# Kernel tuning notes

Hardware: AMD Instinct MI355X
Metric: run time of the kernel (lower is better)

## Reference

```python
import jax, jax.numpy as jnp
import numpy as np
from jax import lax

B_IDX = 0  # label_vocab['B']
E_IDX = 1  # label_vocab['E']
NEG = -10000.0


def setup_inputs() -> dict:
    key = jax.random.key(0)
    k1, k2 = jax.random.split(key)
    B, T, L = 256, 512, 64
    X = jax.random.normal(k1, (B, T, L), dtype=jnp.float32)
    transition = jax.random.normal(k2, (L, L), dtype=jnp.float32)
    # __init__ masking: no transitions out of 'E', none into 'B'
    transition = transition.at[E_IDX, :].set(NEG)
    transition = transition.at[:, B_IDX].set(NEG)
    return {"X": X, "transition": transition}


def reference(X, transition):
    # CRF forward (alpha) recursion, vectorized over the tag dimension and
    # batched; recurrence over timesteps carried by lax.scan.
    B, T, L = X.shape
    init_alpha = jnp.full((B, L), NEG, dtype=X.dtype).at[:, B_IDX].set(0.0)

    def step(alpha, x_t):
        # alpha: [B, L] (prev tag), x_t: [B, L] (emission for next tag)
        # next_var[b, prev, nxt] = alpha[b, prev] + transition[prev, nxt] + x_t[b, nxt]
        next_var = alpha[:, :, None] + transition[None, :, :] + x_t[:, None, :]
        new_alpha = jax.nn.logsumexp(next_var, axis=1)  # reduce over prev tag
        return new_alpha, None

    X_tbl = jnp.moveaxis(X, 1, 0)  # [T, B, L]
    final_alpha, _ = lax.scan(step, init_alpha, X_tbl)
    return final_alpha  # [B, L]
```

## Files before the change

kernel.cpp:

```cpp
#include <hip/hip_runtime.h>

#define LTAG 64
#define NEGV -10000.0f
#define L2E 1.4426950408889634f
#define LN2 0.6931471805599453f

__device__ __forceinline__ float exp2_fast(float x) { return __builtin_amdgcn_exp2f(x); }
__device__ __forceinline__ float log2_fast(float x) { return __builtin_amdgcn_logf(x); }

__device__ __forceinline__ float readlane_f(float v, int lane) {
    return __int_as_float(__builtin_amdgcn_readlane(__float_as_int(v), lane));
}

__global__ __launch_bounds__(64) void crf_forward_kernel(
    const float* __restrict__ X, const float* __restrict__ trans,
    float* __restrict__ out, int T) {
    const int lane = threadIdx.x;
    const int b = blockIdx.x;
    const float* xb = X + (size_t)b * T * LTAG + lane;

    __shared__ __align__(16) float e_sh[LTAG];

    float etr[LTAG];
    float c2 = -3.0e38f;
#pragma unroll
    for (int p = 0; p < LTAG; ++p) {
        etr[p] = trans[p * LTAG + lane] * L2E;
        c2 = fmaxf(c2, etr[p]);
    }
#pragma unroll
    for (int p = 0; p < LTAG; ++p) etr[p] = exp2_fast(etr[p] - c2);

    float a2 = (lane == 0) ? 0.0f : NEGV * L2E;

    float xr[4];
#pragma unroll
    for (int i = 0; i < 4; ++i) xr[i] = xb[(size_t)i * LTAG];

    for (int t = 0; t < T; t += 4) {
#pragma unroll
        for (int u = 0; u < 4; ++u) {
            const float xcur = xr[u];
            int tpf = t + u + 4;
            tpf = tpf < T ? tpf : T - 1;
            xr[u] = xb[(size_t)tpf * LTAG];

            float m = readlane_f(a2, 0);
            m = fmaxf(m, readlane_f(a2, 2));
            m = fmaxf(m, readlane_f(a2, 19));
            m = fmaxf(m, readlane_f(a2, 37));
            m = fmaxf(m, readlane_f(a2, 53));

            e_sh[lane] = exp2_fast(a2 - m);
            __syncthreads();

            float s0 = 0.f, s1 = 0.f, s2 = 0.f, s3 = 0.f;
#pragma unroll
            for (int i = 0; i < LTAG / 4; ++i) {
                const float4 ev = *(const float4*)(e_sh + 4 * i);
                s0 = fmaf(ev.x, etr[4 * i + 0], s0);
                s1 = fmaf(ev.y, etr[4 * i + 1], s1);
                s2 = fmaf(ev.z, etr[4 * i + 2], s2);
                s3 = fmaf(ev.w, etr[4 * i + 3], s3);
            }
            const float s = (s0 + s1) + (s2 + s3);
            a2 = fmaf(xcur, L2E, m + c2 + log2_fast(s));
            __syncthreads();
        }
    }

    out[b * LTAG + lane] = a2 * LN2;
}

extern "C" void kernel_launch(void* const* d_in, const int* in_sizes, int n_in,
                              void* d_out, int out_size, void* d_ws, size_t ws_size,
                              hipStream_t stream) {
    const float* X = (const float*)d_in[0];
    const float* trans = (const float*)d_in[1];
    float* out = (float*)d_out;

    const int B = out_size / LTAG;
    const int T = in_sizes[0] / (B * LTAG);

    crf_forward_kernel<<<B, LTAG, 0, stream>>>(X, trans, out, T);
}
```

Before: 211.8 us.

## Recast CRF forward recursion as bf16 MFMA matmul in linear space over 16 batches

Replaces the per-batch log-space recursion with a linear-space formulation where each wave processes 16 batch rows and computes exp(alpha)·exp(trans) with bf16 MFMA instructions. Rescaling happens only every fourth step via exponent extraction, and the accumulated shift is tracked separately. The B operand is reshuffled with ds_bpermute instead of shared memory and barriers, and the final step is done in fp32. This trades numerical precision (bf16 operands, possible underflow or overflow between rescales) for far fewer scalar FMAs and syncs, but launches only B/16 blocks.

```diff
diff --git a/kernel.cpp b/kernel.cpp
--- a/kernel.cpp
+++ b/kernel.cpp
@@ -1,75 +1,188 @@
 #include <hip/hip_runtime.h>
 
 #define LTAG 64
-#define NEGV -10000.0f
+#define BPB 16
 #define L2E 1.4426950408889634f
 #define LN2 0.6931471805599453f
 
+typedef float f32x4v __attribute__((ext_vector_type(4)));
+typedef short s16x8 __attribute__((ext_vector_type(8)));
+typedef int i32x4 __attribute__((ext_vector_type(4)));
+
 __device__ __forceinline__ float exp2_fast(float x) { return __builtin_amdgcn_exp2f(x); }
 __device__ __forceinline__ float log2_fast(float x) { return __builtin_amdgcn_logf(x); }
-
-__device__ __forceinline__ float readlane_f(float v, int lane) {
-    return __int_as_float(__builtin_amdgcn_readlane(__float_as_int(v), lane));
+__device__ __forceinline__ int bperm_i(int abytes, int v) {
+    return __builtin_amdgcn_ds_bpermute(abytes, v);
+}
+__device__ __forceinline__ int pack_bf16(float lo, float hi) {
+    const unsigned ul = __float_as_uint(lo) + 0x8000u;
+    const unsigned uh = __float_as_uint(hi) + 0x8000u;
+    return (int)((ul >> 16) | (uh & 0xffff0000u));
+}
+__device__ __forceinline__ float bf16_lo(int w) { return __int_as_float(w << 16); }
+__device__ __forceinline__ float bf16_hi(int w) {
+    return __int_as_float((int)((unsigned)w & 0xffff0000u));
 }
 
 __global__ __launch_bounds__(64) void crf_forward_kernel(
     const float* __restrict__ X, const float* __restrict__ trans,
     float* __restrict__ out, int T) {
     const int lane = threadIdx.x;
-    const int b = blockIdx.x;
-    const float* xb = X + (size_t)b * T * LTAG + lane;
+    const int c = lane & 15;
+    const int g = lane >> 4;
+    const int b0 = blockIdx.x * BPB;
+    const size_t bstr = (size_t)T * LTAG;
+    const float* xc = X + (size_t)(b0 + c) * bstr;
 
-    __shared__ __align__(16) float e_sh[LTAG];
+    i32x4 Af[4][2];
+#pragma unroll
+    for (int RT = 0; RT < 4; ++RT)
+#pragma unroll
+        for (int KS = 0; KS < 2; ++KS) {
+            int q[4];
+#pragma unroll
+            for (int i = 0; i < 4; ++i) {
+                const int k0 = 32 * KS + 8 * g + 2 * i;
+                const int m = 16 * RT + c;
+                q[i] = pack_bf16(exp2_fast(trans[k0 * LTAG + m] * L2E),
+                                 exp2_fast(trans[(k0 + 1) * LTAG + m] * L2E));
+            }
+            Af[RT][KS] = (i32x4){q[0], q[1], q[2], q[3]};
+        }
 
-    float etr[LTAG];
-    float c2 = -3.0e38f;
+    i32x4 Bf[2];
 #pragma unroll
-    for (int p = 0; p < LTAG; ++p) {
-        etr[p] = trans[p * LTAG + lane] * L2E;
-        c2 = fmaxf(c2, etr[p]);
-    }
+    for (int KS = 0; KS < 2; ++KS) {
+        int q[4];
 #pragma unroll
-    for (int p = 0; p < LTAG; ++p) etr[p] = exp2_fast(etr[p] - c2);
-
-    float a2 = (lane == 0) ? 0.0f : NEGV * L2E;
-
-    float xr[4];
-#pragma unroll
-    for (int i = 0; i < 4; ++i) xr[i] = xb[(size_t)i * LTAG];
-
-    for (int t = 0; t < T; t += 4) {
-#pragma unroll
-        for (int u = 0; u < 4; ++u) {
-            const float xcur = xr[u];
-            int tpf = t + u + 4;
-            tpf = tpf < T ? tpf : T - 1;
-            xr[u] = xb[(size_t)tpf * LTAG];
-
-            float m = readlane_f(a2, 0);
-            m = fmaxf(m, readlane_f(a2, 2));
-            m = fmaxf(m, readlane_f(a2, 19));
-            m = fmaxf(m, readlane_f(a2, 37));
-            m = fmaxf(m, readlane_f(a2, 53));
-
-            e_sh[lane] = exp2_fast(a2 - m);
-            __syncthreads();
-
-            float s0 = 0.f, s1 = 0.f, s2 = 0.f, s3 = 0.f;
-#pragma unroll
-            for (int i = 0; i < LTAG / 4; ++i) {
-                const float4 ev = *(const float4*)(e_sh + 4 * i);
-                s0 = fmaf(ev.x, etr[4 * i + 0], s0);
-                s1 = fmaf(ev.y, etr[4 * i + 1], s1);
-                s2 = fmaf(ev.z, etr[4 * i + 2], s2);
-                s3 = fmaf(ev.w, etr[4 * i + 3], s3);
-            }
-            const float s = (s0 + s1) + (s2 + s3);
-            a2 = fmaf(xcur, L2E, m + c2 + log2_fast(s));
-            __syncthreads();
+        for (int i = 0; i < 4; ++i) {
+            const int k0 = 32 * KS + 8 * g + 2 * i;
+            q[i] = pack_bf16(exp2_fast((trans[k0] + xc[k0]) * L2E),
+                             exp2_fast((trans[k0 + 1] + xc[k0 + 1]) * L2E));
         }
+        Bf[KS] = (i32x4){q[0], q[1], q[2], q[3]};
     }
 
-    out[b * LTAG + lane] = a2 * LN2;
+    f32x4v xr0[4], xr1[4], xr2[4], xr3[4];
+#pragma unroll
+    for (int RT = 0; RT < 4; ++RT) {
+        xr0[RT] = *(const f32x4v*)(xc + (size_t)1 * LTAG + 16 * RT + 4 * g);
+        xr1[RT] = *(const f32x4v*)(xc + (size_t)2 * LTAG + 16 * RT + 4 * g);
+        xr2[RT] = *(const f32x4v*)(xc + (size_t)3 * LTAG + 16 * RT + 4 * g);
+        xr3[RT] = *(const f32x4v*)(xc + (size_t)4 * LTAG + 16 * RT + 4 * g);
+    }
+
+    const int adrA = ((((2 * g) & 3) << 4) | c) << 2;
+    const int adrB = ((((2 * g + 1) & 3) << 4) | c) << 2;
+    float SH = 0.0f;
+
+#define SUBSTEP(t_, XR, RESC)                                                 \
+    {                                                                         \
+                                    \
+        f32x4v acc[4];                                                        \
+        _Pragma("unroll") for (int RT = 0; RT < 4; ++RT) {                    \
+            f32x4v z = {0.f, 0.f, 0.f, 0.f};                                  \
+            z = __builtin_amdgcn_mfma_f32_16x16x32_bf16(                      \
+                __builtin_bit_cast(s16x8, Af[RT][0]),                         \
+                __builtin_bit_cast(s16x8, Bf[0]), z, 0, 0, 0);                \
+            acc[RT] = __builtin_amdgcn_mfma_f32_16x16x32_bf16(                \
+                __builtin_bit_cast(s16x8, Af[RT][1]),                         \
+                __builtin_bit_cast(s16x8, Bf[1]), z, 0, 0, 0);                \
+        }                                                                     \
+              \
+        _Pragma("unroll") for (int RT = 0; RT < 4; ++RT)                      \
+        _Pragma("unroll") for (int j = 0; j < 4; ++j)                         \
+            acc[RT][j] *= exp2_fast(XR[RT][j] * L2E);                         \
+                              \
+        {                                                                     \
+            int tp = (t_) + 4;                                                \
+            tp = tp < T ? tp : T - 1;                                         \
+            _Pragma("unroll") for (int RT = 0; RT < 4; ++RT)                  \
+                XR[RT] = *(const f32x4v*)(xc + (size_t)tp * LTAG + 16 * RT +  \
+                                          4 * g);                             \
+        }                                                                     \
+        if (RESC) {                                                           \
+              \
+            float m = acc[0][0];                                              \
+            _Pragma("unroll") for (int RT = 0; RT < 4; ++RT)                  \
+            _Pragma("unroll") for (int j = 0; j < 4; ++j)                     \
+                m = fmaxf(m, acc[RT][j]);                                     \
+            m = fmaxf(m, __shfl_xor(m, 16));                                  \
+            m = fmaxf(m, __shfl_xor(m, 32));                                  \
+            int eb = (__float_as_int(m) >> 23) & 0xff;                        \
+            eb = eb < 1 ? 1 : (eb > 254 ? 254 : eb);    \
+            const float fac = __int_as_float((254 - eb) << 23);               \
+            _Pragma("unroll") for (int RT = 0; RT < 4; ++RT)                  \
+            _Pragma("unroll") for (int j = 0; j < 4; ++j) acc[RT][j] *= fac;  \
+            SH += (float)(eb - 127);                                          \
+        }                                                                     \
+                                     \
+        int pk[4][2];                                                         \
+        _Pragma("unroll") for (int RT = 0; RT < 4; ++RT) {                    \
+            pk[RT][0] = pack_bf16(acc[RT][0], acc[RT][1]);                    \
+            pk[RT][1] = pack_bf16(acc[RT][2], acc[RT][3]);                    \
+        }                                                                     \
+        _Pragma("unroll") for (int KS = 0; KS < 2; ++KS) {                    \
+            const int ra0 = bperm_i(adrA, pk[2 * KS][0]);                     \
+            const int ra1 = bperm_i(adrA, pk[2 * KS][1]);                     \
+            const int ra2 = bperm_i(adrA, pk[2 * KS + 1][0]);                 \
+            const int ra3 = bperm_i(adrA, pk[2 * KS + 1][1]);                 \
+            const int rb0 = bperm_i(adrB, pk[2 * KS][0]);                     \
+            const int rb1 = bperm_i(adrB, pk[2 * KS][1]);                     \
+            const int rb2 = bperm_i(adrB, pk[2 * KS + 1][0]);                 \
+            const int rb3 = bperm_i(adrB, pk[2 * KS + 1][1]);                 \
+            const bool hi = g >= 2;              \
+            Bf[KS] = (i32x4){hi ? ra2 : ra0, hi ? ra3 : ra1,                  \
+                             hi ? rb2 : rb0, hi ? rb3 : rb1};                 \
+        }                                                                     \
+    }
+
+    int t = 1;
+    for (; t + 3 <= T - 2; t += 4) {
+        SUBSTEP(t + 0, xr0, false);
+        SUBSTEP(t + 1, xr1, false);
+        SUBSTEP(t + 2, xr2, false);
+        SUBSTEP(t + 3, xr3, true);
+    }
+    if (t <= T - 2) { SUBSTEP(t, xr0, ((t & 3) == 0)); ++t; }
+    if (t <= T - 2) { SUBSTEP(t, xr1, ((t & 3) == 0)); ++t; }
+    if (t <= T - 2) { SUBSTEP(t, xr2, ((t & 3) == 0)); ++t; }
+#undef SUBSTEP
+
+    __shared__ __align__(16) short vl[BPB][80];
+    __shared__ float shl[BPB];
+#pragma unroll
+    for (int KS = 0; KS < 2; ++KS)
+        *(i32x4*)(&vl[c][32 * KS + 8 * g]) = Bf[KS];
+    shl[c] = SH;
+    __syncthreads();
+
+    const int n = lane;
+    float c2n = -3.0e38f;
+#pragma unroll
+    for (int p = 0; p < LTAG; ++p)
+        c2n = fmaxf(c2n, trans[p * LTAG + n] * L2E);
+    float er[LTAG];
+#pragma unroll
+    for (int p = 0; p < LTAG; ++p)
+        er[p] = exp2_fast(trans[p * LTAG + n] * L2E - c2n);
+
+    for (int b = 0; b < BPB; ++b) {
+        float s0 = 0.f, s1 = 0.f, s2 = 0.f, s3 = 0.f;
+#pragma unroll
+        for (int p = 0; p < LTAG; p += 4) {
+            const int w0 = *(const int*)(&vl[b][p]);
+            const int w1 = *(const int*)(&vl[b][p + 2]);
+            s0 = fmaf(bf16_lo(w0), er[p + 0], s0);
+            s1 = fmaf(bf16_hi(w0), er[p + 1], s1);
+            s2 = fmaf(bf16_lo(w1), er[p + 2], s2);
+            s3 = fmaf(bf16_hi(w1), er[p + 3], s3);
+        }
+        float s = (s0 + s1) + (s2 + s3);
+        s = fmaxf(s, 1e-30f);
+        const float xl = X[(size_t)(b0 + b) * bstr + (size_t)(T - 1) * LTAG + n];
+        out[(b0 + b) * LTAG + n] = (log2_fast(s) + fmaf(xl, L2E, c2n) + shl[b]) * LN2;
+    }
 }
 
 extern "C" void kernel_launch(void* const* d_in, const int* in_sizes, int n_in,
@@ -82,5 +195,5 @@
     const int B = out_size / LTAG;
     const int T = in_sizes[0] / (B * LTAG);
 
-    crf_forward_kernel<<<B, LTAG, 0, stream>>>(X, trans, out, T);
+    crf_forward_kernel<<<B / BPB, 64, 0, stream>>>(X, trans, out, T);
 }
```

New measurement: 251.9 us. 19.0% more time.
